# Kernel tuning notes

Hardware: AMD Instinct MI355X
Metric: run time of the kernel (lower is better)

The kernel has to match this reference:

```python
import jax, jax.numpy as jnp
import numpy as np

# --- constants matching init_kwargs / input_specs ---
B, T, N, C = 16, 60, 196, 512
SEGS, TOP_K, TOP_M = 10, 6, 12
HEADS = 4
HD = C // HEADS  # 128
CLIP = T // SEGS  # 6
FRAMES = CLIP * TOP_K  # 36
LN_EPS = 1e-5


def setup_inputs() -> dict:
    key = jax.random.key(0)
    ks = jax.random.split(key, 16)
    s = 0.02
    return {
        "audio_feat": jax.random.normal(ks[0], (B, T, C), jnp.float32),
        "patch_feat": jax.random.normal(ks[1], (B, T, N, C), jnp.float32),
        "qst_feat": jax.random.normal(ks[2], (B, C), jnp.float32),
        "top_k_index_sort": jnp.sort(jax.random.randint(ks[3], (B, 1, TOP_K), 0, SEGS), axis=-1),
        # MultiheadAttention params (torch layout: in_proj [3C, C])
        "in_proj_w": jax.random.normal(ks[4], (3 * C, C), jnp.float32) * s,
        "in_proj_b": jnp.zeros((3 * C,), jnp.float32),
        "out_w": jax.random.normal(ks[5], (C, C), jnp.float32) * s,
        "out_b": jnp.zeros((C,), jnp.float32),
        # FFN
        "lin1_w": jax.random.normal(ks[6], (C, C), jnp.float32) * s,
        "lin1_b": jnp.zeros((C,), jnp.float32),
        "lin2_w": jax.random.normal(ks[7], (C, C), jnp.float32) * s,
        "lin2_b": jnp.zeros((C,), jnp.float32),
        # LayerNorm
        "ln_g": jnp.ones((C,), jnp.float32),
        "ln_b": jnp.zeros((C,), jnp.float32),
    }


def _layernorm(x, g, b):
    mu = jnp.mean(x, axis=-1, keepdims=True)
    var = jnp.mean(jnp.square(x - mu), axis=-1, keepdims=True)
    return (x - mu) * jax.lax.rsqrt(var + LN_EPS) * g + b


def _forward(audio_feat, patch_feat, qst_feat, top_k_index_sort,
             in_proj_w, in_proj_b, out_w, out_b,
             lin1_w, lin1_b, lin2_w, lin2_b, ln_g, ln_b):
    # --- TopKSegs: gather top-k temporal segments (clip_len frames each) ---
    seg_idx = top_k_index_sort[:, 0, :]  # [B, K]
    frame_ids = (seg_idx[:, :, None] * CLIP + jnp.arange(CLIP)[None, None, :]).reshape(B, FRAMES)
    audio_top_k = jnp.take_along_axis(audio_feat, frame_ids[:, :, None], axis=1)            # [B, F, C]
    patch_top_k = jnp.take_along_axis(patch_feat, frame_ids[:, :, None, None], axis=1)      # [B, F, N, C]

    # --- QstQueryPatchAttn: batched cross-attention (q_len=1 per frame) ---
    Wq, Wk, Wv = in_proj_w[:C], in_proj_w[C:2 * C], in_proj_w[2 * C:]
    bq, bk, bv = in_proj_b[:C], in_proj_b[C:2 * C], in_proj_b[2 * C:]
    q = (qst_feat @ Wq.T + bq).reshape(B, HEADS, HD)                    # [B, h, d]
    k = (patch_top_k @ Wk.T + bk).reshape(B, FRAMES, N, HEADS, HD)      # [B, F, N, h, d]
    v = (patch_top_k @ Wv.T + bv).reshape(B, FRAMES, N, HEADS, HD)
    scale = 1.0 / jnp.sqrt(jnp.asarray(HD, jnp.float32))
    scores = jnp.einsum('bhd,bfnhd->bfhn', q, k) * scale                # [B, F, h, N]
    w = jax.nn.softmax(scores, axis=-1)
    ctx = jnp.einsum('bfhn,bfnhd->bfhd', w, v).reshape(B, FRAMES, C)
    attn_feat = ctx @ out_w.T + out_b                                   # [B, F, C]
    patch_weights = jnp.mean(w, axis=2)                                 # [B, F, N] (avg heads)

    src = jax.nn.relu(attn_feat @ lin1_w.T + lin1_b) @ lin2_w.T + lin2_b
    visual_spatial_feat = _layernorm(attn_feat + src, ln_g, ln_b)       # computed but unused downstream

    # --- SelectTopM (faithful to original loop semantics):
    # top-m indices are sorted ascending and iterated with full-slab overwrite,
    sort_index = jnp.argsort(patch_weights, axis=-1)
    top_m_index = sort_index[:, :, -TOP_M:]
    top_m_index_sort = jnp.sort(top_m_index, axis=-1)
    pid = top_m_index_sort[0, 0, -1]  # last iterated patch id
    sel = jnp.take(patch_top_k, pid, axis=2)                            # [B, F, C]
    visual_patch_top_m = jnp.broadcast_to(sel[:, :, None, :], (B, FRAMES, TOP_M, C))
    visual_patch_feat = visual_patch_top_m.reshape(B, FRAMES * TOP_M, C)
    return audio_top_k, visual_patch_top_m, visual_patch_feat


def reference(audio_feat, patch_feat, qst_feat, top_k_index_sort,
              in_proj_w, in_proj_b, out_w, out_b,
              lin1_w, lin1_b, lin2_w, lin2_b, ln_g, ln_b):
    return _forward(audio_feat, patch_feat, qst_feat, top_k_index_sort,
                    in_proj_w, in_proj_b, out_w, out_b,
                    lin1_w, lin1_b, lin2_w, lin2_b, ln_g, ln_b)
```

## Files before the change

kernel.cpp:

```cpp
#include <hip/hip_runtime.h>
#include <math.h>

#define B_     16
#define T_     60
#define N_     196
#define C_     512
#define SEGS_  10
#define TOPK_  6
#define TOPM_  12
#define HEADS_ 4
#define HD_    128
#define CLIP_  6
#define FRAMES_ 36

#define WS_Q   0
#define WS_SC  512
#define WS_PID 1296

#define SCALE_ 0.08838834764831845f

__global__ void qproj_kernel(const float* __restrict__ qst,
                             const float* __restrict__ ipw,
                             const float* __restrict__ ipb,
                             float* __restrict__ ws) {
    __shared__ float x[C_];
    int tid = threadIdx.x;
    x[tid]       = qst[tid];
    x[tid + 256] = qst[tid + 256];
    __syncthreads();
    const float4* x4 = (const float4*)x;
    for (int r = tid; r < C_; r += 256) {
        const float4* w4 = (const float4*)(ipw + (size_t)r * C_);
        float acc = 0.f;
        #pragma unroll 8
        for (int c = 0; c < C_ / 4; ++c) {
            float4 wv = w4[c], xv = x4[c];
            acc += wv.x * xv.x + wv.y * xv.y + wv.z * xv.z + wv.w * xv.w;
        }
        ws[WS_Q + r] = acc + ipb[r];
    }
}

#define NPER 4
__global__ void score_kernel(const float* __restrict__ patch,
                             const int* __restrict__ tk,
                             const float* __restrict__ ipw,
                             const float* __restrict__ ipb,
                             float* __restrict__ ws) {
    __shared__ float xs[NPER][C_];
    __shared__ float qs[C_];
    __shared__ float kb[NPER][C_];
    int tid = threadIdx.x;
    int n0 = blockIdx.x * NPER;
    int fid0 = tk[0] * CLIP_;
    const size_t base = (size_t)fid0 * N_ * C_;

    qs[tid]       = ws[WS_Q + tid];
    qs[tid + 256] = ws[WS_Q + tid + 256];
    for (int i = tid; i < NPER * C_; i += 256) {
        int n = i >> 9, c = i & (C_ - 1);
        xs[n][c] = patch[base + (size_t)(n0 + n) * C_ + c];
    }
    __syncthreads();

    float a0 = 0.f, a1 = 0.f, a2 = 0.f, a3 = 0.f;
    float b0 = 0.f, b1 = 0.f, b2 = 0.f, b3 = 0.f;
    {
        const float4* w0 = (const float4*)(ipw + (size_t)(C_ + tid) * C_);
        const float4* w1 = (const float4*)(ipw + (size_t)(C_ + tid + 256) * C_);
        const float4* x0 = (const float4*)xs[0];
        const float4* x1 = (const float4*)xs[1];
        const float4* x2 = (const float4*)xs[2];
        const float4* x3 = (const float4*)xs[3];
        for (int c = 0; c < C_ / 4; ++c) {
            float4 wa = w0[c], wb = w1[c];
            float4 v0 = x0[c], v1 = x1[c], v2 = x2[c], v3 = x3[c];
            a0 += wa.x * v0.x + wa.y * v0.y + wa.z * v0.z + wa.w * v0.w;
            a1 += wa.x * v1.x + wa.y * v1.y + wa.z * v1.z + wa.w * v1.w;
            a2 += wa.x * v2.x + wa.y * v2.y + wa.z * v2.z + wa.w * v2.w;
            a3 += wa.x * v3.x + wa.y * v3.y + wa.z * v3.z + wa.w * v3.w;
            b0 += wb.x * v0.x + wb.y * v0.y + wb.z * v0.z + wb.w * v0.w;
            b1 += wb.x * v1.x + wb.y * v1.y + wb.z * v1.z + wb.w * v1.w;
            b2 += wb.x * v2.x + wb.y * v2.y + wb.z * v2.z + wb.w * v2.w;
            b3 += wb.x * v3.x + wb.y * v3.y + wb.z * v3.z + wb.w * v3.w;
        }
    }
    float bk0 = ipb[C_ + tid];
    float bk1 = ipb[C_ + tid + 256];
    kb[0][tid] = a0 + bk0; kb[1][tid] = a1 + bk0;
    kb[2][tid] = a2 + bk0; kb[3][tid] = a3 + bk0;
    kb[0][tid + 256] = b0 + bk1; kb[1][tid + 256] = b1 + bk1;
    kb[2][tid + 256] = b2 + bk1; kb[3][tid + 256] = b3 + bk1;
    __syncthreads();

    int h = tid >> 6, j = tid & 63;
    for (int nn = 0; nn < NPER; ++nn) {
        float p = qs[h * HD_ + j]      * kb[nn][h * HD_ + j]
                + qs[h * HD_ + 64 + j] * kb[nn][h * HD_ + 64 + j];
        for (int off = 32; off; off >>= 1) p += __shfl_down(p, off);
        if (j == 0) ws[WS_SC + h * N_ + n0 + nn] = p * SCALE_;
    }
}

__global__ void pid_kernel(float* __restrict__ ws) {
    __shared__ float wgt[HEADS_][N_];
    __shared__ float pw[N_];
    int tid = threadIdx.x;
    int h = tid >> 6, j = tid & 63;

    float sc[4]; float ex[4];
    int m = 0;
    float mx = -1e30f;
    for (int n = j; n < N_; n += 64) {
        sc[m] = ws[WS_SC + h * N_ + n];
        mx = fmaxf(mx, sc[m]);
        ++m;
    }
    for (int off = 1; off < 64; off <<= 1) mx = fmaxf(mx, __shfl_xor(mx, off));
    float sum = 0.f;
    for (int s = 0; s < m; ++s) { ex[s] = expf(sc[s] - mx); sum += ex[s]; }
    for (int off = 1; off < 64; off <<= 1) sum += __shfl_xor(sum, off);
    float inv = 1.f / sum;
    m = 0;
    for (int n = j; n < N_; n += 64) { wgt[h][n] = ex[m] * inv; ++m; }
    __syncthreads();

    for (int n = tid; n < N_; n += 256)
        pw[n] = 0.25f * (wgt[0][n] + wgt[1][n] + wgt[2][n] + wgt[3][n]);
    __syncthreads();

    if (tid < 64) {
        float v[4];
        for (int s = 0; s < 4; ++s) {
            int n = j + 64 * s;
            v[s] = (n < N_) ? pw[n] : -1e30f;
        }
        int pid = -1;
        for (int r = 0; r < TOPM_; ++r) {
            float bv = -1e30f; int bi = -1;
            for (int s = 0; s < 4; ++s) {
                int n = j + 64 * s;
                if (v[s] > bv || (v[s] == bv && n > bi)) { bv = v[s]; bi = n; }
            }
            for (int off = 1; off < 64; off <<= 1) {
                float ov = __shfl_xor(bv, off);
                int   oi = __shfl_xor(bi, off);
                if (ov > bv || (ov == bv && oi > bi)) { bv = ov; bi = oi; }
            }
            if ((bi & 63) == j) v[bi >> 6] = -1e30f;
            if (bi > pid) pid = bi;
        }
        if (j == 0) ((int*)ws)[WS_PID] = pid;
    }
}

__global__ void out_kernel(const float* __restrict__ audio,
                           const float* __restrict__ patch,
                           const int* __restrict__ tk,
                           const float* __restrict__ ws,
                           float* __restrict__ out) {
    int bf = blockIdx.x;
    int b = bf / FRAMES_, f = bf % FRAMES_;
    int k = f / CLIP_, c = f % CLIP_;
    int fid = tk[b * TOPK_ + k] * CLIP_ + c;
    int t = threadIdx.x;
    int pid = ((const int*)ws)[WS_PID];

    const float4* a4 = (const float4*)(audio + ((size_t)b * T_ + fid) * C_);
    const float4* p4 = (const float4*)(patch + (((size_t)b * T_ + fid) * N_ + pid) * C_);
    float4 av = a4[t];
    float4 sv = p4[t];

    float4* o0 = (float4*)out;
    float4* o1 = (float4*)(out + (size_t)B_ * FRAMES_ * C_);
    float4* o2 = (float4*)(out + (size_t)B_ * FRAMES_ * C_ + (size_t)B_ * FRAMES_ * TOPM_ * C_);

    o0[(size_t)bf * (C_ / 4) + t] = av;
    size_t rb = (size_t)bf * TOPM_ * (C_ / 4);
    #pragma unroll
    for (int mm = 0; mm < TOPM_; ++mm) {
        o1[rb + mm * (C_ / 4) + t] = sv;
        o2[rb + mm * (C_ / 4) + t] = sv;
    }
}

extern "C" void kernel_launch(void* const* d_in, const int* in_sizes, int n_in,
                              void* d_out, int out_size, void* d_ws, size_t ws_size,
                              hipStream_t stream) {
    const float* audio = (const float*)d_in[0];
    const float* patch = (const float*)d_in[1];
    const float* qst   = (const float*)d_in[2];
    const int*   tk    = (const int*)d_in[3];
    const float* ipw   = (const float*)d_in[4];
    const float* ipb   = (const float*)d_in[5];
    float* out = (float*)d_out;
    float* ws  = (float*)d_ws;

    qproj_kernel<<<1, 256, 0, stream>>>(qst, ipw, ipb, ws);
    score_kernel<<<N_ / NPER, 256, 0, stream>>>(patch, tk, ipw, ipb, ws);
    pid_kernel<<<1, 256, 0, stream>>>(ws);
    out_kernel<<<B_ * FRAMES_, 128, 0, stream>>>(audio, patch, tk, ws, out);
}
```

Baseline: 527.9 us.

## Fuse query projection into score kernel and top-M selection into output kernel

Removes the separate single-block query-projection and pid kernels. Each score block now recomputes the query projection redundantly alongside its key projection. Every output block redundantly recomputes softmax, head averaging and top-M selection with one wavefront before writing. This cuts two launches and two serial single-block stages, at the cost of extra redundant weight reads and per-block work in the 576 output blocks.

```diff
diff --git a/kernel.cpp b/kernel.cpp
--- a/kernel.cpp
+++ b/kernel.cpp
@@ -5,7 +5,6 @@
 #define T_     60
 #define N_     196
 #define C_     512
-#define SEGS_  10
 #define TOPK_  6
 #define TOPM_  12
 #define HEADS_ 4
@@ -13,40 +12,18 @@
 #define CLIP_  6
 #define FRAMES_ 36
 
-#define WS_Q   0
-#define WS_SC  512
-#define WS_PID 1296
+#define WS_SC  0
 
 #define SCALE_ 0.08838834764831845f
 
-__global__ void qproj_kernel(const float* __restrict__ qst,
-                             const float* __restrict__ ipw,
-                             const float* __restrict__ ipb,
-                             float* __restrict__ ws) {
-    __shared__ float x[C_];
-    int tid = threadIdx.x;
-    x[tid]       = qst[tid];
-    x[tid + 256] = qst[tid + 256];
-    __syncthreads();
-    const float4* x4 = (const float4*)x;
-    for (int r = tid; r < C_; r += 256) {
-        const float4* w4 = (const float4*)(ipw + (size_t)r * C_);
-        float acc = 0.f;
-        #pragma unroll 8
-        for (int c = 0; c < C_ / 4; ++c) {
-            float4 wv = w4[c], xv = x4[c];
-            acc += wv.x * xv.x + wv.y * xv.y + wv.z * xv.z + wv.w * xv.w;
-        }
-        ws[WS_Q + r] = acc + ipb[r];
-    }
-}
-
 #define NPER 4
 __global__ void score_kernel(const float* __restrict__ patch,
+                             const float* __restrict__ qst,
                              const int* __restrict__ tk,
                              const float* __restrict__ ipw,
                              const float* __restrict__ ipb,
                              float* __restrict__ ws) {
+    __shared__ float xq[C_];
     __shared__ float xs[NPER][C_];
     __shared__ float qs[C_];
     __shared__ float kb[NPER][C_];
@@ -55,25 +32,33 @@
     int fid0 = tk[0] * CLIP_;
     const size_t base = (size_t)fid0 * N_ * C_;
 
-    qs[tid]       = ws[WS_Q + tid];
-    qs[tid + 256] = ws[WS_Q + tid + 256];
+    xq[tid]       = qst[tid];
+    xq[tid + 256] = qst[tid + 256];
     for (int i = tid; i < NPER * C_; i += 256) {
         int n = i >> 9, c = i & (C_ - 1);
         xs[n][c] = patch[base + (size_t)(n0 + n) * C_ + c];
     }
     __syncthreads();
 
+    float q0 = 0.f, q1 = 0.f;
     float a0 = 0.f, a1 = 0.f, a2 = 0.f, a3 = 0.f;
     float b0 = 0.f, b1 = 0.f, b2 = 0.f, b3 = 0.f;
     {
-        const float4* w0 = (const float4*)(ipw + (size_t)(C_ + tid) * C_);
-        const float4* w1 = (const float4*)(ipw + (size_t)(C_ + tid + 256) * C_);
+        const float4* wq0 = (const float4*)(ipw + (size_t)tid * C_);
+        const float4* wq1 = (const float4*)(ipw + (size_t)(tid + 256) * C_);
+        const float4* wk0 = (const float4*)(ipw + (size_t)(C_ + tid) * C_);
+        const float4* wk1 = (const float4*)(ipw + (size_t)(C_ + tid + 256) * C_);
+        const float4* q4 = (const float4*)xq;
         const float4* x0 = (const float4*)xs[0];
         const float4* x1 = (const float4*)xs[1];
         const float4* x2 = (const float4*)xs[2];
         const float4* x3 = (const float4*)xs[3];
         for (int c = 0; c < C_ / 4; ++c) {
-            float4 wa = w0[c], wb = w1[c];
+            float4 ra = wq0[c], rb = wq1[c];
+            float4 qv = q4[c];
+            q0 += ra.x * qv.x + ra.y * qv.y + ra.z * qv.z + ra.w * qv.w;
+            q1 += rb.x * qv.x + rb.y * qv.y + rb.z * qv.z + rb.w * qv.w;
+            float4 wa = wk0[c], wb = wk1[c];
             float4 v0 = x0[c], v1 = x1[c], v2 = x2[c], v3 = x3[c];
             a0 += wa.x * v0.x + wa.y * v0.y + wa.z * v0.z + wa.w * v0.w;
             a1 += wa.x * v1.x + wa.y * v1.y + wa.z * v1.z + wa.w * v1.w;
@@ -85,6 +70,8 @@
             b3 += wb.x * v3.x + wb.y * v3.y + wb.z * v3.z + wb.w * v3.w;
         }
     }
+    qs[tid]       = q0 + ipb[tid];
+    qs[tid + 256] = q1 + ipb[tid + 256];
     float bk0 = ipb[C_ + tid];
     float bk1 = ipb[C_ + tid + 256];
     kb[0][tid] = a0 + bk0; kb[1][tid] = a1 + bk0;
@@ -102,38 +89,36 @@
     }
 }
 
-__global__ void pid_kernel(float* __restrict__ ws) {
-    __shared__ float wgt[HEADS_][N_];
-    __shared__ float pw[N_];
+__global__ void out_kernel(const float* __restrict__ audio,
+                           const float* __restrict__ patch,
+                           const int* __restrict__ tk,
+                           const float* __restrict__ ws,
+                           float* __restrict__ out) {
+    __shared__ int pid_s;
     int tid = threadIdx.x;
-    int h = tid >> 6, j = tid & 63;
-
-    float sc[4]; float ex[4];
-    int m = 0;
-    float mx = -1e30f;
-    for (int n = j; n < N_; n += 64) {
-        sc[m] = ws[WS_SC + h * N_ + n];
-        mx = fmaxf(mx, sc[m]);
-        ++m;
-    }
-    for (int off = 1; off < 64; off <<= 1) mx = fmaxf(mx, __shfl_xor(mx, off));
-    float sum = 0.f;
-    for (int s = 0; s < m; ++s) { ex[s] = expf(sc[s] - mx); sum += ex[s]; }
-    for (int off = 1; off < 64; off <<= 1) sum += __shfl_xor(sum, off);
-    float inv = 1.f / sum;
-    m = 0;
-    for (int n = j; n < N_; n += 64) { wgt[h][n] = ex[m] * inv; ++m; }
-    __syncthreads();
-
-    for (int n = tid; n < N_; n += 256)
-        pw[n] = 0.25f * (wgt[0][n] + wgt[1][n] + wgt[2][n] + wgt[3][n]);
-    __syncthreads();
-
     if (tid < 64) {
+        int j = tid;
+        float pwacc[4] = {0.f, 0.f, 0.f, 0.f};
+        for (int h = 0; h < HEADS_; ++h) {
+            float sc[4], ex[4];
+            float mx = -1e30f;
+            int m = 0;
+            for (int n = j; n < N_; n += 64) {
+                sc[m] = ws[WS_SC + h * N_ + n];
+                mx = fmaxf(mx, sc[m]);
+                ++m;
+            }
+            for (int off = 1; off < 64; off <<= 1) mx = fmaxf(mx, __shfl_xor(mx, off));
+            float sum = 0.f;
+            for (int s = 0; s < m; ++s) { ex[s] = expf(sc[s] - mx); sum += ex[s]; }
+            for (int off = 1; off < 64; off <<= 1) sum += __shfl_xor(sum, off);
+            float inv = 1.f / sum;
+            for (int s = 0; s < m; ++s) pwacc[s] += ex[s] * inv;
+        }
         float v[4];
         for (int s = 0; s < 4; ++s) {
             int n = j + 64 * s;
-            v[s] = (n < N_) ? pw[n] : -1e30f;
+            v[s] = (n < N_) ? 0.25f * pwacc[s] : -1e30f;
         }
         int pid = -1;
         for (int r = 0; r < TOPM_; ++r) {
@@ -150,21 +135,16 @@
             if ((bi & 63) == j) v[bi >> 6] = -1e30f;
             if (bi > pid) pid = bi;
         }
-        if (j == 0) ((int*)ws)[WS_PID] = pid;
+        if (j == 0) pid_s = pid;
     }
-}
+    __syncthreads();
+    int pid = pid_s;
 
-__global__ void out_kernel(const float* __restrict__ audio,
-                           const float* __restrict__ patch,
-                           const int* __restrict__ tk,
-                           const float* __restrict__ ws,
-                           float* __restrict__ out) {
     int bf = blockIdx.x;
     int b = bf / FRAMES_, f = bf % FRAMES_;
     int k = f / CLIP_, c = f % CLIP_;
     int fid = tk[b * TOPK_ + k] * CLIP_ + c;
-    int t = threadIdx.x;
-    int pid = ((const int*)ws)[WS_PID];
+    int t = tid;
 
     const float4* a4 = (const float4*)(audio + ((size_t)b * T_ + fid) * C_);
     const float4* p4 = (const float4*)(patch + (((size_t)b * T_ + fid) * N_ + pid) * C_);
@@ -196,8 +176,6 @@
     float* out = (float*)d_out;
     float* ws  = (float*)d_ws;
 
-    qproj_kernel<<<1, 256, 0, stream>>>(qst, ipw, ipb, ws);
-    score_kernel<<<N_ / NPER, 256, 0, stream>>>(patch, tk, ipw, ipb, ws);
-    pid_kernel<<<1, 256, 0, stream>>>(ws);
+    score_kernel<<<N_ / NPER, 256, 0, stream>>>(patch, qst, tk, ipw, ipb, ws);
     out_kernel<<<B_ * FRAMES_, 128, 0, stream>>>(audio, patch, tk, ws, out);
 }
```

Result: no change. 533.7 us (+1.1%).
